# Kernel tuning notes

Hardware: AMD Instinct MI355X
Metric: run time of the kernel (lower is better)

The kernel has to match this reference:

```python
import jax, jax.numpy as jnp
import numpy as np

N = 50000      # nodes
E = 800000     # edges (avg degree 16)
IN = 128       # in_channels
OUT = 64       # out_channels
HID = 2 * OUT  # 128, hidden width of conv1
EPS = 1e-5     # BatchNorm eps


def _edge_norm(edge_index):
    # PyG ChebConv with sym normalization, lambda_max=2: L_hat = -D^{-1/2} A D^{-1/2}
    src, dst = edge_index[0], edge_index[1]
    deg = jax.ops.segment_sum(jnp.ones((E,), jnp.float32), src, num_segments=N)
    dinv = jnp.where(deg > 0, jax.lax.rsqrt(jnp.maximum(deg, 1.0)), 0.0)
    return -dinv[src] * dinv[dst]


def _cheb(x, src, dst, norm, W0, W1, b):
    # K=2 Chebyshev conv: Tx0 = x, Tx1 = L_hat x (sparse propagate)
    tx1 = jax.ops.segment_sum(x[src] * norm[:, None], dst, num_segments=N)
    return x @ W0 + tx1 @ W1 + b


def setup_inputs() -> dict:
    key = jax.random.key(0)
    ks = jax.random.split(key, 14)
    g = lambda k, shp, fan: jax.random.normal(k, shp, jnp.float32) / np.sqrt(fan)
    return {
        "x": jax.random.normal(ks[0], (N, IN), jnp.float32),
        "edge_index": jax.random.randint(ks[1], (2, E), 0, N, dtype=jnp.int32),
        "W1_0": g(ks[2], (IN, HID), IN),
        "W1_1": g(ks[3], (IN, HID), IN),
        "b1": jnp.zeros((HID,), jnp.float32),
        "gamma": jnp.ones((HID,), jnp.float32),
        "beta": jnp.zeros((HID,), jnp.float32),
        "Wmu_0": g(ks[4], (HID, OUT), HID),
        "Wmu_1": g(ks[5], (HID, OUT), HID),
        "b_mu": jnp.zeros((OUT,), jnp.float32),
        "Wls_0": g(ks[6], (HID, OUT), HID),
        "Wls_1": g(ks[7], (HID, OUT), HID),
        "b_ls": jnp.zeros((OUT,), jnp.float32),
    }


def reference(x, edge_index, W1_0, W1_1, b1, gamma, beta,
              Wmu_0, Wmu_1, b_mu, Wls_0, Wls_1, b_ls):
    src, dst = edge_index[0], edge_index[1]
    norm = _edge_norm(edge_index)
    h = _cheb(x, src, dst, norm, W1_0, W1_1, b1)         # [N, HID]
    # BatchNorm1d (training mode: batch statistics over nodes)
    mean = jnp.mean(h, axis=0)
    var = jnp.var(h, axis=0)
    h = (h - mean) * jax.lax.rsqrt(var + EPS) * gamma + beta
    h = jax.nn.relu(h)
    mu = _cheb(h, src, dst, norm, Wmu_0, Wmu_1, b_mu)    # [N, OUT]
    logstd = _cheb(h, src, dst, norm, Wls_0, Wls_1, b_ls)
    return (mu, logstd)
```

## Files before the change

kernel.cpp:

```cpp
#include <hip/hip_runtime.h>
#include <cstddef>
#include <cstdint>

static constexpr int IN_C  = 128;
static constexpr float BN_EPS = 1e-5f;
static constexpr int OUT_C = 64;

static constexpr int CS_C = 32;
static constexpr int CS_R = 8;
static constexpr int CS_RANGE = 6250;

using bf16x8 = __attribute__((ext_vector_type(8))) short;
using f32x4  = __attribute__((ext_vector_type(4))) float;

__device__ __forceinline__ ushort f2bf(float f) {
    uint u = __float_as_uint(f);
    u += 0x7fffu + ((u >> 16) & 1u);
    return (ushort)(u >> 16);
}
__device__ __forceinline__ uint pack2(float a, float b) {
    return (uint)f2bf(a) | ((uint)f2bf(b) << 16);
}
__device__ __forceinline__ float bf_lo(uint v) { return __uint_as_float(v << 16); }
__device__ __forceinline__ float bf_hi(uint v) { return __uint_as_float(v & 0xffff0000u); }

__device__ __forceinline__ int swz8(int row, int g) { return (g ^ ((row >> 1) & 3)) * 8; }

__global__ __launch_bounds__(1024) void hist_conv_k(
    const int* __restrict__ src, const int* __restrict__ dst,
    ushort* __restrict__ hsrc_part, ushort* __restrict__ hdst_part,
    int N, int E, int chunk, int range, int nb_hist, int nb_x,
    const float* __restrict__ x, ushort* __restrict__ xb,
    const float* __restrict__ W1_0, const float* __restrict__ W1_1,
    const float* __restrict__ b1,
    const float* __restrict__ Wmu_0, const float* __restrict__ Wmu_1,
    const float* __restrict__ b_mu,
    const float* __restrict__ Wls_0, const float* __restrict__ Wls_1,
    const float* __restrict__ b_ls,
    ushort* __restrict__ Wt1, ushort* __restrict__ Wt2,
    float* __restrict__ bias1, float* __restrict__ bias2) {
    __shared__ int hs_[CS_RANGE];
    __shared__ int hd_[CS_RANGE];
    int bid = blockIdx.x;
    if (bid < nb_hist) {
        int c = bid & (CS_C - 1);
        int r = bid / CS_C;
        int base = r * range;
        int hi = min(base + range, N);
        int rsz = hi - base;
        for (int j = threadIdx.x; j < rsz; j += 1024) { hs_[j] = 0; hd_[j] = 0; }
        __syncthreads();
        int e0 = c * chunk, e1 = min(e0 + chunk, E);
        for (int i = e0 + threadIdx.x; i < e1; i += 1024) {
            int s = src[i];
            if (s >= base && s < hi) atomicAdd(&hs_[s - base], 1);
            int t = dst[i];
            if (t >= base && t < hi) atomicAdd(&hd_[t - base], 1);
        }
        __syncthreads();
        for (int j = threadIdx.x; j < rsz; j += 1024) {
            hsrc_part[(size_t)c * N + base + j] = (ushort)hs_[j];
            hdst_part[(size_t)c * N + base + j] = (ushort)hd_[j];
        }
    } else if (bid < nb_hist + nb_x) {
        int i = (bid - nb_hist) * 1024 + threadIdx.x;
        if (i < N * 64) {
            float2 v = ((const float2*)x)[i];
            ((uint*)xb)[i] = pack2(v.x, v.y);
        }
    } else {
        int idx = (bid - nb_hist - nb_x) * 1024 + threadIdx.x;
        int which = idx >> 15;
        int c = (idx >> 8) & 127;
        int k = idx & 255;
        if (which == 0) {
            float v = (k < 128) ? W1_0[k * 128 + c] : W1_1[(k - 128) * 128 + c];
            Wt1[c * 256 + k] = f2bf(v);
            if (k == 0) bias1[c] = b1[c];
        } else {
            float v;
            if (c < 64) v = (k < 128) ? Wmu_0[k * 64 + c] : Wmu_1[(k - 128) * 64 + c];
            else        v = (k < 128) ? Wls_0[k * 64 + (c - 64)] : Wls_1[(k - 128) * 64 + (c - 64)];
            Wt2[c * 256 + k] = f2bf(v);
            if (k == 0) bias2[c] = (c < 64) ? b_mu[c] : b_ls[c - 64];
        }
    }
}

__global__ __launch_bounds__(256) void count_k(
    const ushort* __restrict__ hsrc_part, const ushort* __restrict__ hdst_part,
    float* __restrict__ dinv, int* __restrict__ cnt_dst,
    int* __restrict__ bsum, float* __restrict__ stats, int N) {
    __shared__ int sw[4];
    int tid = threadIdx.x;
    if (blockIdx.x == 0) stats[tid] = 0.f;
    int v = blockIdx.x * 256 + tid;
    int b = 0;
    if (v < N) {
        int a = 0;
        for (int c = 0; c < CS_C; ++c) {
            a += hsrc_part[(size_t)c * N + v];
            b += hdst_part[(size_t)c * N + v];
        }
        dinv[v] = (a > 0) ? rsqrtf((float)a) : 0.f;
        cnt_dst[v] = b;
    }
    int t = b;
    #pragma unroll
    for (int off = 1; off < 64; off <<= 1) t += __shfl_xor(t, off, 64);
    if ((tid & 63) == 0) sw[tid >> 6] = t;
    __syncthreads();
    if (tid == 0) bsum[blockIdx.x] = sw[0] + sw[1] + sw[2] + sw[3];
}

__global__ __launch_bounds__(256) void phase3_k(
    const int* __restrict__ cnt, const int* __restrict__ bsum,
    int* __restrict__ row_ptr, const ushort* __restrict__ hdst_part,
    int* __restrict__ offs, int n, int nb) {
    __shared__ int sbp[4];
    __shared__ int swv[4];
    int tid = threadIdx.x;
    int lane = tid & 63, wave = tid >> 6;
    int bv = (tid < nb && tid < (int)blockIdx.x) ? bsum[tid] : 0;
    int t = bv;
    #pragma unroll
    for (int off = 1; off < 64; off <<= 1) t += __shfl_xor(t, off, 64);
    if (lane == 0) sbp[wave] = t;
    int v = blockIdx.x * 256 + tid;
    int c = (v < n) ? cnt[v] : 0;
    int s = c;
    #pragma unroll
    for (int off = 1; off < 64; off <<= 1) {
        int u = __shfl_up(s, off, 64);
        if (lane >= off) s += u;
    }
    if (lane == 63) swv[wave] = s;
    __syncthreads();
    int bpre = sbp[0] + sbp[1] + sbp[2] + sbp[3];
    int wexcl = 0;
    for (int w = 0; w < wave; ++w) wexcl += swv[w];
    int st = bpre + wexcl + (s - c);
    if (v < n) row_ptr[v + 1] = st + c;
    if (v == 0) row_ptr[0] = 0;
    int r = st;
    for (int ch = 0; ch < CS_C; ++ch) {
        size_t idx = (size_t)ch * n + v;
        if (v < n) {
            offs[idx] = r;
            r += hdst_part[idx];
        }
    }
}

__global__ __launch_bounds__(1024) void scatter_k(
    const int* __restrict__ src, const int* __restrict__ dst,
    const int* __restrict__ off, int* __restrict__ col,
    int N, int E, int chunk, int range) {
    __shared__ int cur[CS_RANGE];
    int c = blockIdx.x & (CS_C - 1);
    int r = blockIdx.x / CS_C;
    int base = r * range;
    int hi = min(base + range, N);
    int rsz = hi - base;
    for (int j = threadIdx.x; j < rsz; j += 1024)
        cur[j] = off[(size_t)c * N + base + j];
    __syncthreads();
    int e0 = c * chunk, e1 = min(e0 + chunk, E);
    for (int i = e0 + threadIdx.x; i < e1; i += 1024) {
        int t = dst[i];
        if (t >= base && t < hi) {
            int pos = atomicAdd(&cur[t - base], 1);
            col[pos] = src[i];
        }
    }
}

#define FMA8(V, D)                                                 \
    acc[0] += bf_lo((V).x) * (D); acc[1] += bf_hi((V).x) * (D);    \
    acc[2] += bf_lo((V).y) * (D); acc[3] += bf_hi((V).y) * (D);    \
    acc[4] += bf_lo((V).z) * (D); acc[5] += bf_hi((V).z) * (D);    \
    acc[6] += bf_lo((V).w) * (D); acc[7] += bf_hi((V).w) * (D);

__global__ __launch_bounds__(256) void propagate4_k(
    const uint4* __restrict__ xs, uint4* __restrict__ out,
    const int* __restrict__ row_ptr, const int* __restrict__ col,
    const float* __restrict__ dinv, int n) {
    int wid = (blockIdx.x * 256 + threadIdx.x) >> 6;
    if (wid >= n) return;
    int lane = threadIdx.x & 63;
    int g = lane >> 4, li = lane & 15;
    int s = row_ptr[wid], e = row_ptr[wid + 1];
    float acc[8];
    #pragma unroll
    for (int k = 0; k < 8; ++k) acc[k] = 0.f;
    int i = s + g;
    for (; i + 12 < e; i += 16) {
        int c0 = col[i];
        int c1 = col[i + 4];
        int c2 = col[i + 8];
        int c3 = col[i + 12];
        float d0 = dinv[c0], d1 = dinv[c1], d2 = dinv[c2], d3 = dinv[c3];
        uint4 v0 = xs[(size_t)c0 * 16 + li];
        uint4 v1 = xs[(size_t)c1 * 16 + li];
        uint4 v2 = xs[(size_t)c2 * 16 + li];
        uint4 v3 = xs[(size_t)c3 * 16 + li];
        FMA8(v0, d0); FMA8(v1, d1); FMA8(v2, d2); FMA8(v3, d3);
    }
    for (; i < e; i += 4) {
        int c0 = col[i];
        float d0 = dinv[c0];
        uint4 v0 = xs[(size_t)c0 * 16 + li];
        FMA8(v0, d0);
    }
    #pragma unroll
    for (int k = 0; k < 8; ++k) {
        acc[k] += __shfl_xor(acc[k], 16, 64);
        acc[k] += __shfl_xor(acc[k], 32, 64);
    }
    if (g == 0) {
        float sc = -dinv[wid];
        uint4 o;
        o.x = pack2(acc[0] * sc, acc[1] * sc);
        o.y = pack2(acc[2] * sc, acc[3] * sc);
        o.z = pack2(acc[4] * sc, acc[5] * sc);
        o.w = pack2(acc[6] * sc, acc[7] * sc);
        out[(size_t)wid * 16 + li] = o;
    }
}

template <int MODE>
__global__ __launch_bounds__(256) void gemm_mfma_k(
    const ushort* __restrict__ A0, const ushort* __restrict__ A1,
    const ushort* __restrict__ Wt, const float* __restrict__ bias,
    ushort* __restrict__ Cb, float* __restrict__ Cmu, float* __restrict__ Cls,
    float* __restrict__ stats, int n) {
    __shared__ ushort sA[64][32];
    __shared__ ushort sW[128][32];
    __shared__ float smS[4][128];
    __shared__ float smQ[4][128];

    int tid = threadIdx.x;
    int block_row = blockIdx.x * 64;
    int wave = tid >> 6, lane = tid & 63;
    int col_base = lane & 15;
    int quad = lane >> 4;
    int m_local = wave * 16 + col_base;

    f32x4 acc[8];
    #pragma unroll
    for (int t = 0; t < 8; ++t) acc[t] = (f32x4){0.f, 0.f, 0.f, 0.f};

    for (int k0 = 0; k0 < 256; k0 += 32) {
        {
            int row = tid >> 2, g = tid & 3;
            int grow = block_row + row;
            int kc = k0 + g * 8;
            uint4 v = make_uint4(0, 0, 0, 0);
            if (grow < n) {
                const ushort* srcp = (kc < 128) ? (A0 + (size_t)grow * 128 + kc)
                                                : (A1 + (size_t)grow * 128 + (kc - 128));
                v = *(const uint4*)srcp;
            }
            *(uint4*)&sA[row][swz8(row, g)] = v;
        }
        #pragma unroll
        for (int i = tid; i < 512; i += 256) {
            int c = i >> 2, g = i & 3;
            *(uint4*)&sW[c][swz8(c, g)] = *(const uint4*)(Wt + (size_t)c * 256 + k0 + g * 8);
        }
        __syncthreads();
        bf16x8 af = *(const bf16x8*)&sA[m_local][swz8(m_local, quad)];
        #pragma unroll
        for (int t = 0; t < 8; ++t) {
            int wr = t * 16 + col_base;
            bf16x8 bfr = *(const bf16x8*)&sW[wr][swz8(wr, quad)];
            acc[t] = __builtin_amdgcn_mfma_f32_16x16x32_bf16(af, bfr, acc[t], 0, 0, 0);
        }
        __syncthreads();
    }

    int row_l = wave * 16 + quad * 4;
    #pragma unroll
    for (int t = 0; t < 8; ++t) {
        int col = t * 16 + col_base;
        float b = bias[col];
        float s = 0.f, q = 0.f;
        #pragma unroll
        for (int r = 0; r < 4; ++r) {
            int grow = block_row + row_l + r;
            if (grow < n) {
                float v = acc[t][r] + b;
                if (MODE == 0) {
                    Cb[(size_t)grow * 128 + col] = f2bf(v);
                    s += v; q += v * v;
                } else {
                    if (col < 64) Cmu[(size_t)grow * 64 + col] = v;
                    else          Cls[(size_t)grow * 64 + (col - 64)] = v;
                }
            }
        }
        if (MODE == 0) {
            s += __shfl_xor(s, 16, 64); s += __shfl_xor(s, 32, 64);
            q += __shfl_xor(q, 16, 64); q += __shfl_xor(q, 32, 64);
            if (quad == 0) { smS[wave][col] = s; smQ[wave][col] = q; }
        }
    }
    if (MODE == 0) {
        __syncthreads();
        if (tid < 128) {
            float s = smS[0][tid] + smS[1][tid] + smS[2][tid] + smS[3][tid];
            float q = smQ[0][tid] + smQ[1][tid] + smQ[2][tid] + smQ[3][tid];
            atomicAdd(&stats[tid], s);
            atomicAdd(&stats[128 + tid], q);
        }
    }
}

__global__ __launch_bounds__(256) void bn_apply_k(
    ushort* __restrict__ hb, const float* __restrict__ stats,
    const float* __restrict__ gamma, const float* __restrict__ beta,
    float inv_n, int n64) {
    __shared__ float sp[256];
    int tid = threadIdx.x;
    if (tid < 128) {
        float mean = stats[tid] * inv_n;
        float var = stats[128 + tid] * inv_n - mean * mean;
        float sc = gamma[tid] * rsqrtf(var + BN_EPS);
        sp[tid] = sc;
        sp[128 + tid] = beta[tid] - mean * sc;
    }
    __syncthreads();
    int i = blockIdx.x * 256 + tid;
    if (i >= n64) return;
    int c2 = (i & 63) * 2;
    uint v = ((uint*)hb)[i];
    float f0 = fmaxf(bf_lo(v) * sp[c2]     + sp[128 + c2],     0.f);
    float f1 = fmaxf(bf_hi(v) * sp[c2 + 1] + sp[128 + c2 + 1], 0.f);
    ((uint*)hb)[i] = pack2(f0, f1);
}

extern "C" void kernel_launch(void* const* d_in, const int* in_sizes, int n_in,
                              void* d_out, int out_size, void* d_ws, size_t ws_size,
                              hipStream_t stream) {
    const float* x = (const float*)d_in[0];
    const int* edge_index = (const int*)d_in[1];
    const float* W1_0 = (const float*)d_in[2];
    const float* W1_1 = (const float*)d_in[3];
    const float* b1 = (const float*)d_in[4];
    const float* gamma = (const float*)d_in[5];
    const float* beta = (const float*)d_in[6];
    const float* Wmu_0 = (const float*)d_in[7];
    const float* Wmu_1 = (const float*)d_in[8];
    const float* b_mu = (const float*)d_in[9];
    const float* Wls_0 = (const float*)d_in[10];
    const float* Wls_1 = (const float*)d_in[11];
    const float* b_ls = (const float*)d_in[12];

    const int N = in_sizes[0] / IN_C;
    const int E = in_sizes[1] / 2;
    const int* src = edge_index;
    const int* dst = edge_index + E;

    char* w = (char*)d_ws;
    auto alloc = [&](size_t bytes) {
        char* p = w;
        w += (bytes + 15) & ~(size_t)15;
        return p;
    };
    float* stats = (float*)alloc(256 * 4);
    int* row_ptr = (int*)alloc((size_t)(N + 1) * 4);
    int* bsum    = (int*)alloc(256 * 4);
    float* dinv  = (float*)alloc((size_t)N * 4);
    int* cnt_dst = (int*)alloc((size_t)N * 4);
    int* col     = (int*)alloc((size_t)E * 4);
    ushort* hsrc_part = (ushort*)alloc((size_t)CS_C * N * 2);
    ushort* hdst_part = (ushort*)alloc((size_t)CS_C * N * 2);
    int* offs    = (int*)alloc((size_t)CS_C * N * 4);
    ushort* x_bf  = (ushort*)alloc((size_t)N * 128 * 2);
    ushort* xp_bf = (ushort*)alloc((size_t)N * 128 * 2);
    ushort* h_bf  = (ushort*)alloc((size_t)N * 128 * 2);
    ushort* Wt1   = (ushort*)alloc(128 * 256 * 2);
    ushort* Wt2   = (ushort*)alloc(128 * 256 * 2);
    float* bias1  = (float*)alloc(128 * 4);
    float* bias2  = (float*)alloc(128 * 4);

    float* out_mu = (float*)d_out;
    float* out_ls = out_mu + (size_t)N * OUT_C;

    int chunk = (E + CS_C - 1) / CS_C;
    int range = (N + CS_R - 1) / CS_R;
    int NBLK = (N + 255) / 256;
    int nb_hist = CS_R * CS_C;
    int nb_x = (N * 64 + 1023) / 1024;
    int nb_w = 64;

    hist_conv_k<<<nb_hist + nb_x + nb_w, 1024, 0, stream>>>(
        src, dst, hsrc_part, hdst_part, N, E, chunk, range, nb_hist, nb_x,
        x, x_bf, W1_0, W1_1, b1, Wmu_0, Wmu_1, b_mu, Wls_0, Wls_1, b_ls,
        Wt1, Wt2, bias1, bias2);
    count_k<<<NBLK, 256, 0, stream>>>(hsrc_part, hdst_part, dinv, cnt_dst, bsum, stats, N);
    phase3_k<<<NBLK, 256, 0, stream>>>(cnt_dst, bsum, row_ptr, hdst_part, offs, N, NBLK);
    scatter_k<<<nb_hist, 1024, 0, stream>>>(src, dst, offs, col, N, E, chunk, range);

    int pb = (N + 3) / 4;
    propagate4_k<<<pb, 256, 0, stream>>>((const uint4*)x_bf, (uint4*)xp_bf,
                                         row_ptr, col, dinv, N);

    int gb = (N + 63) / 64;
    gemm_mfma_k<0><<<gb, 256, 0, stream>>>(x_bf, xp_bf, Wt1, bias1, h_bf,
                                           nullptr, nullptr, stats, N);

    bn_apply_k<<<(N * 64 + 255) / 256, 256, 0, stream>>>(h_bf, stats, gamma, beta,
                                                         1.f / (float)N, N * 64);

    propagate4_k<<<pb, 256, 0, stream>>>((const uint4*)h_bf, (uint4*)xp_bf,
                                         row_ptr, col, dinv, N);

    gemm_mfma_k<1><<<gb, 256, 0, stream>>>(h_bf, xp_bf, Wt2, bias2, nullptr,
                                           out_mu, out_ls, stats, N);
}
```

Before: 279.5 us.

## Fuse BatchNorm+ReLU into second propagate gather and GEMM A-load

Removes the standalone BN-apply kernel. BN scale/shift and ReLU are now applied on the fly to gathered neighbor rows in the second propagate and to the A0 tile loads in the second GEMM. This avoids a full read-modify-write pass over the hidden activations and one launch. In exchange, it recomputes the affine+ReLU per edge in the gather, which adds ALU work, and every block recomputes BN parameters.

```diff
diff --git a/kernel.cpp b/kernel.cpp
--- a/kernel.cpp
+++ b/kernel.cpp
@@ -175,20 +175,47 @@
     }
 }
 
-#define FMA8(V, D)                                                 \
-    acc[0] += bf_lo((V).x) * (D); acc[1] += bf_hi((V).x) * (D);    \
-    acc[2] += bf_lo((V).y) * (D); acc[3] += bf_hi((V).y) * (D);    \
-    acc[4] += bf_lo((V).z) * (D); acc[5] += bf_hi((V).z) * (D);    \
-    acc[6] += bf_lo((V).w) * (D); acc[7] += bf_hi((V).w) * (D);
-
+#define FMA8(V, D)                                                            \
+  { float v0_ = bf_lo((V).x), v1_ = bf_hi((V).x), v2_ = bf_lo((V).y),         \
+          v3_ = bf_hi((V).y), v4_ = bf_lo((V).z), v5_ = bf_hi((V).z),         \
+          v6_ = bf_lo((V).w), v7_ = bf_hi((V).w);                             \
+    if (BN) {                                                                 \
+      v0_ = fmaxf(v0_ * sc[0] + sh[0], 0.f);                                  \
+      v1_ = fmaxf(v1_ * sc[1] + sh[1], 0.f);                                  \
+      v2_ = fmaxf(v2_ * sc[2] + sh[2], 0.f);                                  \
+      v3_ = fmaxf(v3_ * sc[3] + sh[3], 0.f);                                  \
+      v4_ = fmaxf(v4_ * sc[4] + sh[4], 0.f);                                  \
+      v5_ = fmaxf(v5_ * sc[5] + sh[5], 0.f);                                  \
+      v6_ = fmaxf(v6_ * sc[6] + sh[6], 0.f);                                  \
+      v7_ = fmaxf(v7_ * sc[7] + sh[7], 0.f);                                  \
+    }                                                                         \
+    acc[0] += v0_ * (D); acc[1] += v1_ * (D); acc[2] += v2_ * (D);            \
+    acc[3] += v3_ * (D); acc[4] += v4_ * (D); acc[5] += v5_ * (D);            \
+    acc[6] += v6_ * (D); acc[7] += v7_ * (D); }
+
+template <int BN>
 __global__ __launch_bounds__(256) void propagate4_k(
     const uint4* __restrict__ xs, uint4* __restrict__ out,
     const int* __restrict__ row_ptr, const int* __restrict__ col,
-    const float* __restrict__ dinv, int n) {
+    const float* __restrict__ dinv, int n,
+    const float* __restrict__ stats, const float* __restrict__ gamma,
+    const float* __restrict__ beta, float inv_n) {
     int wid = (blockIdx.x * 256 + threadIdx.x) >> 6;
     if (wid >= n) return;
     int lane = threadIdx.x & 63;
     int g = lane >> 4, li = lane & 15;
+    float sc[8], sh[8];
+    if (BN) {
+        #pragma unroll
+        for (int j = 0; j < 8; ++j) {
+            int f = li * 8 + j;
+            float mean = stats[f] * inv_n;
+            float var = stats[128 + f] * inv_n - mean * mean;
+            float s = gamma[f] * rsqrtf(var + BN_EPS);
+            sc[j] = s;
+            sh[j] = beta[f] - mean * s;
+        }
+    }
     int s = row_ptr[wid], e = row_ptr[wid + 1];
     float acc[8];
     #pragma unroll
@@ -218,12 +245,12 @@
         acc[k] += __shfl_xor(acc[k], 32, 64);
     }
     if (g == 0) {
-        float sc = -dinv[wid];
+        float scl = -dinv[wid];
         uint4 o;
-        o.x = pack2(acc[0] * sc, acc[1] * sc);
-        o.y = pack2(acc[2] * sc, acc[3] * sc);
-        o.z = pack2(acc[4] * sc, acc[5] * sc);
-        o.w = pack2(acc[6] * sc, acc[7] * sc);
+        o.x = pack2(acc[0] * scl, acc[1] * scl);
+        o.y = pack2(acc[2] * scl, acc[3] * scl);
+        o.z = pack2(acc[4] * scl, acc[5] * scl);
+        o.w = pack2(acc[6] * scl, acc[7] * scl);
         out[(size_t)wid * 16 + li] = o;
     }
 }
@@ -233,11 +260,14 @@
     const ushort* __restrict__ A0, const ushort* __restrict__ A1,
     const ushort* __restrict__ Wt, const float* __restrict__ bias,
     ushort* __restrict__ Cb, float* __restrict__ Cmu, float* __restrict__ Cls,
-    float* __restrict__ stats, int n) {
+    float* __restrict__ stats, int n,
+    const float* __restrict__ gamma, const float* __restrict__ beta,
+    float inv_n) {
     __shared__ ushort sA[64][32];
     __shared__ ushort sW[128][32];
     __shared__ float smS[4][128];
     __shared__ float smQ[4][128];
+    __shared__ float sp[256];
 
     int tid = threadIdx.x;
     int block_row = blockIdx.x * 64;
@@ -245,6 +275,17 @@
     int col_base = lane & 15;
     int quad = lane >> 4;
     int m_local = wave * 16 + col_base;
+
+    if (MODE == 1) {
+        if (tid < 128) {
+            float mean = stats[tid] * inv_n;
+            float var = stats[128 + tid] * inv_n - mean * mean;
+            float s = gamma[tid] * rsqrtf(var + BN_EPS);
+            sp[tid] = s;
+            sp[128 + tid] = beta[tid] - mean * s;
+        }
+        __syncthreads();
+    }
 
     f32x4 acc[8];
     #pragma unroll
@@ -260,6 +301,18 @@
                 const ushort* srcp = (kc < 128) ? (A0 + (size_t)grow * 128 + kc)
                                                 : (A1 + (size_t)grow * 128 + (kc - 128));
                 v = *(const uint4*)srcp;
+                if (MODE == 1 && kc < 128) {
+                    float a0 = fmaxf(bf_lo(v.x) * sp[kc + 0] + sp[128 + kc + 0], 0.f);
+                    float a1 = fmaxf(bf_hi(v.x) * sp[kc + 1] + sp[128 + kc + 1], 0.f);
+                    float a2 = fmaxf(bf_lo(v.y) * sp[kc + 2] + sp[128 + kc + 2], 0.f);
+                    float a3 = fmaxf(bf_hi(v.y) * sp[kc + 3] + sp[128 + kc + 3], 0.f);
+                    float a4 = fmaxf(bf_lo(v.z) * sp[kc + 4] + sp[128 + kc + 4], 0.f);
+                    float a5 = fmaxf(bf_hi(v.z) * sp[kc + 5] + sp[128 + kc + 5], 0.f);
+                    float a6 = fmaxf(bf_lo(v.w) * sp[kc + 6] + sp[128 + kc + 6], 0.f);
+                    float a7 = fmaxf(bf_hi(v.w) * sp[kc + 7] + sp[128 + kc + 7], 0.f);
+                    v.x = pack2(a0, a1); v.y = pack2(a2, a3);
+                    v.z = pack2(a4, a5); v.w = pack2(a6, a7);
+                }
             }
             *(uint4*)&sA[row][swz8(row, g)] = v;
         }
@@ -314,29 +367,6 @@
             atomicAdd(&stats[128 + tid], q);
         }
     }
-}
-
-__global__ __launch_bounds__(256) void bn_apply_k(
-    ushort* __restrict__ hb, const float* __restrict__ stats,
-    const float* __restrict__ gamma, const float* __restrict__ beta,
-    float inv_n, int n64) {
-    __shared__ float sp[256];
-    int tid = threadIdx.x;
-    if (tid < 128) {
-        float mean = stats[tid] * inv_n;
-        float var = stats[128 + tid] * inv_n - mean * mean;
-        float sc = gamma[tid] * rsqrtf(var + BN_EPS);
-        sp[tid] = sc;
-        sp[128 + tid] = beta[tid] - mean * sc;
-    }
-    __syncthreads();
-    int i = blockIdx.x * 256 + tid;
-    if (i >= n64) return;
-    int c2 = (i & 63) * 2;
-    uint v = ((uint*)hb)[i];
-    float f0 = fmaxf(bf_lo(v) * sp[c2]     + sp[128 + c2],     0.f);
-    float f1 = fmaxf(bf_hi(v) * sp[c2 + 1] + sp[128 + c2 + 1], 0.f);
-    ((uint*)hb)[i] = pack2(f0, f1);
 }
 
 extern "C" void kernel_launch(void* const* d_in, const int* in_sizes, int n_in,
@@ -393,6 +423,7 @@
     int nb_hist = CS_R * CS_C;
     int nb_x = (N * 64 + 1023) / 1024;
     int nb_w = 64;
+    float inv_n = 1.f / (float)N;
 
     hist_conv_k<<<nb_hist + nb_x + nb_w, 1024, 0, stream>>>(
         src, dst, hsrc_part, hdst_part, N, E, chunk, range, nb_hist, nb_x,
@@ -403,19 +434,20 @@
     scatter_k<<<nb_hist, 1024, 0, stream>>>(src, dst, offs, col, N, E, chunk, range);
 
     int pb = (N + 3) / 4;
-    propagate4_k<<<pb, 256, 0, stream>>>((const uint4*)x_bf, (uint4*)xp_bf,
-                                         row_ptr, col, dinv, N);
+    propagate4_k<0><<<pb, 256, 0, stream>>>((const uint4*)x_bf, (uint4*)xp_bf,
+                                            row_ptr, col, dinv, N,
+                                            nullptr, nullptr, nullptr, 0.f);
 
     int gb = (N + 63) / 64;
     gemm_mfma_k<0><<<gb, 256, 0, stream>>>(x_bf, xp_bf, Wt1, bias1, h_bf,
-                                           nullptr, nullptr, stats, N);
-
-    bn_apply_k<<<(N * 64 + 255) / 256, 256, 0, stream>>>(h_bf, stats, gamma, beta,
-                                                         1.f / (float)N, N * 64);
-
-    propagate4_k<<<pb, 256, 0, stream>>>((const uint4*)h_bf, (uint4*)xp_bf,
-                                         row_ptr, col, dinv, N);
+                                           nullptr, nullptr, stats, N,
+                                           nullptr, nullptr, 0.f);
+
+    propagate4_k<1><<<pb, 256, 0, stream>>>((const uint4*)h_bf, (uint4*)xp_bf,
+                                            row_ptr, col, dinv, N,
+                                            stats, gamma, beta, inv_n);
 
     gemm_mfma_k<1><<<gb, 256, 0, stream>>>(h_bf, xp_bf, Wt2, bias2, nullptr,
-                                           out_mu, out_ls, stats, N);
-}
+                                           out_mu, out_ls, stats, N,
+                                           gamma, beta, inv_n);
+}
```

Result: no change. 279.4 us (-0.0%).
